# Kernel tuning notes

Hardware: AMD Instinct MI355X
Metric: run time of the kernel (lower is better)

Reference implementation:

```python
import jax, jax.numpy as jnp
import numpy as np

N_TOKENS = 8192
HIDDEN = 4096
N_EXPERTS = 64
TOP_K = 8


def setup_inputs() -> dict:
    key = jax.random.key(0)
    k1, k2 = jax.random.split(key)
    h = jax.random.normal(k1, (N_TOKENS, HIDDEN), dtype=jnp.float32)
    weight = jax.random.normal(k2, (N_EXPERTS, HIDDEN), dtype=jnp.float32) * (1.0 / np.sqrt(HIDDEN))
    return {"h": h, "weight": weight}


def reference(h, weight):
    # logits = h @ W^T in fp32  -> [n_tokens, n_experts]
    logits = jnp.einsum("th,eh->te", h.astype(jnp.float32), weight.astype(jnp.float32))
    scores = jax.nn.softmax(logits, axis=-1)
    topk_weight, topk_idx = jax.lax.top_k(scores, TOP_K)  # [n_tokens, k]
    return topk_weight, topk_idx
```

## Files before the change

### kernel.cpp

```cpp
#include <hip/hip_runtime.h>
#include <math.h>
#include <stdint.h>

#define NTOK 8192
#define HID  4096
#define NEXP 64
#define TOPK 8

typedef float    f32x4 __attribute__((ext_vector_type(4)));
typedef _Float16 f16x8 __attribute__((ext_vector_type(8)));


__device__ __forceinline__ void cvt_hilo(f32x4 a, f32x4 b, f16x8& hi, f16x8& lo)
{
    float x[8] = {a.x, a.y, a.z, a.w, b.x, b.y, b.z, b.w};
#pragma unroll
    for (int j = 0; j < 8; ++j) {
        const _Float16 h = (_Float16)x[j];
        hi[j] = h;
        lo[j] = (_Float16)(x[j] - (float)h);
    }
}

__device__ __forceinline__ void gll16(const void* g, void* l) {
    __builtin_amdgcn_global_load_lds(
        (const __attribute__((address_space(1))) uint32_t*)g,
        (__attribute__((address_space(3))) uint32_t*)l, 16, 0, 0);
}

__global__ __launch_bounds__(256)
void k0_wsplit(const float* __restrict__ W, char* __restrict__ wsW)
{
    const int gidx = blockIdx.x * 256 + threadIdx.x;
    const int kt = gidx >> 9;
    const int r  = (gidx >> 3) & 63;
    const int c  = gidx & 7;

    const float* src = W + (size_t)r * HID + kt * 64 + c * 8;
    const f32x4 w0 = *(const f32x4*)src;
    const f32x4 w1 = *(const f32x4*)(src + 4);
    f16x8 hi, lo;
    cvt_hilo(w0 * 2048.0f, w1 * 2048.0f, hi, lo);

    f16x8* tile = (f16x8*)(wsW + (size_t)kt * 16384);
    const int cp = c ^ (r & 7);
    tile[r * 8 + cp]       = hi;
    tile[512 + r * 8 + cp] = lo;
}

#define AL(SET, S) do { const float* _p = ha + (S) * 32;                      \
    SET##0 = *(const f32x4*)_p; SET##1 = *(const f32x4*)(_p + 4); } while (0)

#define STEPU(SET, KS) do {                                                   \
    f16x8 _ah, _al; cvt_hilo(SET##0, SET##1, _ah, _al);                       \
    const int _ci = ((KS) * 4 + kg) ^ (lr & 7);                               \
    _Pragma("unroll")                                                         \
    for (int _e4 = 0; _e4 < 4; ++_e4) {                                       \
        const int _ix = _e4 * 128 + lr * 8 + _ci;                             \
        const f16x8 _bh = *(const f16x8*)&bt[_ix * 8];                        \
        const f16x8 _bl = *(const f16x8*)&bt[4096 + _ix * 8];                 \
        accH[_e4] = __builtin_amdgcn_mfma_f32_16x16x32_f16(_ah, _bh, accH[_e4], 0, 0, 0); \
        accM[_e4] = __builtin_amdgcn_mfma_f32_16x16x32_f16(_ah, _bl, accM[_e4], 0, 0, 0); \
        accL[_e4] = __builtin_amdgcn_mfma_f32_16x16x32_f16(_al, _bh, accL[_e4], 0, 0, 0); \
    } } while (0)

__global__ __launch_bounds__(256, 3)
void k1_partial(const float* __restrict__ Hm, const char* __restrict__ wsW,
                float* __restrict__ lgp)
{
    __shared__ _Float16 B[2][8192];

    const int tid  = threadIdx.x;
    const int wave = tid >> 6;
    const int l    = tid & 63;
    const int lr   = l & 15;
    const int kg   = l >> 4;
    const int tg   = blockIdx.x >> 2;
    const int m    = blockIdx.x & 3;
    const int tok0 = tg * 64 + wave * 16;

    const float* ha = Hm + (size_t)(tok0 + lr) * HID + m * 1024 + kg * 8;
    const char*  wsrc = wsW + (size_t)m * 16 * 16384 + tid * 16;
    const int    ldsoff = wave * 512;

    f32x4 accH[4], accM[4], accL[4];
#pragma unroll
    for (int e = 0; e < 4; ++e) {
        accH[e] = (f32x4)(0.0f); accM[e] = (f32x4)(0.0f); accL[e] = (f32x4)(0.0f);
    }

    f32x4 Aa0, Aa1, Ab0, Ab1;
    AL(Aa, 0); AL(Ab, 1);
#pragma unroll
    for (int i = 0; i < 4; ++i)
        gll16(wsrc + i * 4096, &B[0][i * 2048 + ldsoff]);
    __syncthreads();

#pragma unroll 1
    for (int kt = 0; kt < 16; ++kt) {
        const int p = kt & 1;
        if (kt < 15) {
            const char* s = wsrc + (size_t)(kt + 1) * 16384;
#pragma unroll
            for (int i = 0; i < 4; ++i)
                gll16(s + i * 4096, &B[p ^ 1][i * 2048 + ldsoff]);
        }
        const _Float16* bt = &B[p][0];
        const int S0 = 2 * kt;
        STEPU(Aa, 0); { const int Sn = (S0 + 2 < 32) ? S0 + 2 : 31; AL(Aa, Sn); }
        STEPU(Ab, 1); { const int Sn = (S0 + 3 < 32) ? S0 + 3 : 31; AL(Ab, Sn); }
        __syncthreads();
    }

    float* wsw = lgp + ((size_t)m * NTOK + tok0) * 64;
#pragma unroll
    for (int e4 = 0; e4 < 4; ++e4) {
        const f32x4 a = accH[e4] + accM[e4] + accL[e4];
#pragma unroll
        for (int r = 0; r < 4; ++r)
            wsw[(kg * 4 + r) * 64 + e4 * 16 + lr] = a[r];
    }
}

__global__ __launch_bounds__(256)
void k2_finish(const float* __restrict__ lgp, float* __restrict__ out)
{
    __shared__ __align__(16) float sc[4][64];
    const int tid  = threadIdx.x;
    const int wave = tid >> 6;
    const int lane = tid & 63;
    float* outw = out;
    float* outi = out + (size_t)NTOK * TOPK;

#pragma unroll 1
    for (int t = 0; t < 4; ++t) {
        const int tok = blockIdx.x * 16 + wave * 4 + t;
        const float* p = lgp + (size_t)tok * 64 + lane;
        const float lgv = ((p[0] + p[(size_t)NTOK * 64])
                         + (p[(size_t)2 * NTOK * 64] + p[(size_t)3 * NTOK * 64]))
                         * (1.0f / 2048.0f);

        float mx = lgv;
#pragma unroll
        for (int off = 32; off; off >>= 1) mx = fmaxf(mx, __shfl_xor(mx, off));
        const float pv = expf(lgv - mx);

        sc[wave][lane] = pv;
        __syncthreads();

        float ss = 0.f;
        int rank = 0;
#pragma unroll
        for (int j4 = 0; j4 < 16; ++j4) {
            const f32x4 v = *(const f32x4*)&sc[wave][j4 * 4];
#pragma unroll
            for (int u = 0; u < 4; ++u) {
                const int j = j4 * 4 + u;
                ss += v[u];
                rank += (v[u] > pv || (v[u] == pv && j < lane)) ? 1 : 0;
            }
        }
        if (rank < TOPK) {
            outw[(size_t)tok * TOPK + rank] = pv / ss;
            outi[(size_t)tok * TOPK + rank] = (float)lane;
        }
        __syncthreads();
    }
}

extern "C" void kernel_launch(void* const* d_in, const int* in_sizes, int n_in,
                              void* d_out, int out_size, void* d_ws, size_t ws_size,
                              hipStream_t stream) {
    (void)in_sizes; (void)n_in; (void)out_size; (void)ws_size;
    const float* h = (const float*)d_in[0];
    const float* w = (const float*)d_in[1];
    float* out = (float*)d_out;

    char*  wsW = (char*)d_ws;
    float* lgp = (float*)((char*)d_ws + (1 << 20));

    k0_wsplit<<<128, 256, 0, stream>>>(w, wsW);
    k1_partial<<<512, 256, 0, stream>>>(h, wsW, lgp);
    k2_finish<<<512, 256, 0, stream>>>(lgp, out);
}
```

Measured before the change: 48.60 us.

## Double K-tile depth, fully unroll k1 with deeper A prefetch, one-token-per-wave finish

After: 44.77 us. 1.09x faster.

```diff
diff --git a/kernel.cpp b/kernel.cpp
--- a/kernel.cpp
+++ b/kernel.cpp
@@ -32,43 +32,61 @@
 void k0_wsplit(const float* __restrict__ W, char* __restrict__ wsW)
 {
     const int gidx = blockIdx.x * 256 + threadIdx.x;
-    const int kt = gidx >> 9;
-    const int r  = (gidx >> 3) & 63;
-    const int c  = gidx & 7;
+    const int kt = gidx >> 10;
+    const int r  = (gidx >> 4) & 63;
+    const int sl = gidx & 15;
+    const int c  = sl ^ (r & 7);
 
-    const float* src = W + (size_t)r * HID + kt * 64 + c * 8;
+    const float* src = W + (size_t)r * HID + kt * 128 + c * 8;
     const f32x4 w0 = *(const f32x4*)src;
     const f32x4 w1 = *(const f32x4*)(src + 4);
     f16x8 hi, lo;
     cvt_hilo(w0 * 2048.0f, w1 * 2048.0f, hi, lo);
 
-    f16x8* tile = (f16x8*)(wsW + (size_t)kt * 16384);
-    const int cp = c ^ (r & 7);
-    tile[r * 8 + cp]       = hi;
-    tile[512 + r * 8 + cp] = lo;
+    f16x8* tile = (f16x8*)(wsW + (size_t)kt * 32768);
+    tile[r * 16 + sl]        = hi;
+    tile[1024 + r * 16 + sl] = lo;
 }
 
 #define AL(SET, S) do { const float* _p = ha + (S) * 32;                      \
     SET##0 = *(const f32x4*)_p; SET##1 = *(const f32x4*)(_p + 4); } while (0)
+#define ALG(SET, S) do { if ((S) < 32) AL(SET, S); } while (0)
 
 #define STEPU(SET, KS) do {                                                   \
     f16x8 _ah, _al; cvt_hilo(SET##0, SET##1, _ah, _al);                       \
-    const int _ci = ((KS) * 4 + kg) ^ (lr & 7);                               \
     _Pragma("unroll")                                                         \
     for (int _e4 = 0; _e4 < 4; ++_e4) {                                       \
-        const int _ix = _e4 * 128 + lr * 8 + _ci;                             \
-        const f16x8 _bh = *(const f16x8*)&bt[_ix * 8];                        \
-        const f16x8 _bl = *(const f16x8*)&bt[4096 + _ix * 8];                 \
+        const int _r  = _e4 * 16 + lr;                                        \
+        const int _sl = ((KS) * 4 + kg) ^ (lr & 7);                           \
+        const f16x8 _bh = *(const f16x8*)&bt[(_r * 16 + _sl) * 8];            \
+        const f16x8 _bl = *(const f16x8*)&bt[8192 + (_r * 16 + _sl) * 8];     \
         accH[_e4] = __builtin_amdgcn_mfma_f32_16x16x32_f16(_ah, _bh, accH[_e4], 0, 0, 0); \
         accM[_e4] = __builtin_amdgcn_mfma_f32_16x16x32_f16(_ah, _bl, accM[_e4], 0, 0, 0); \
         accL[_e4] = __builtin_amdgcn_mfma_f32_16x16x32_f16(_al, _bh, accL[_e4], 0, 0, 0); \
     } } while (0)
 
-__global__ __launch_bounds__(256, 3)
+#define STAGE(KT, BUF) do {                                                   \
+    const char* _s = wsrc + (KT) * 32768;                                     \
+    _Pragma("unroll")                                                         \
+    for (int _t = 0; _t < 8; ++_t)                                            \
+        gll16(_s + _t * 4096, (void*)&BT[BUF][_t * 2048 + tid * 8]);          \
+} while (0)
+
+#define KTILE(KT, SA, SB, SC, SD) do {                                        \
+    if ((KT) < 7) STAGE((KT) + 1, ((KT) & 1) ^ 1);                            \
+    const _Float16* bt = &BT[(KT) & 1][0];                                    \
+    STEPU(SA, 0); ALG(SA, (KT) * 4 + 8);                                      \
+    STEPU(SB, 1); ALG(SB, (KT) * 4 + 9);                                      \
+    STEPU(SC, 2); ALG(SC, (KT) * 4 + 10);                                     \
+    STEPU(SD, 3); ALG(SD, (KT) * 4 + 11);                                     \
+    __syncthreads();                                                          \
+} while (0)
+
+__global__ __launch_bounds__(256, 2)
 void k1_partial(const float* __restrict__ Hm, const char* __restrict__ wsW,
                 float* __restrict__ lgp)
 {
-    __shared__ _Float16 B[2][8192];
+    __shared__ _Float16 BT[2][16384];
 
     const int tid  = threadIdx.x;
     const int wave = tid >> 6;
@@ -79,9 +97,8 @@
     const int m    = blockIdx.x & 3;
     const int tok0 = tg * 64 + wave * 16;
 
-    const float* ha = Hm + (size_t)(tok0 + lr) * HID + m * 1024 + kg * 8;
-    const char*  wsrc = wsW + (size_t)m * 16 * 16384 + tid * 16;
-    const int    ldsoff = wave * 512;
+    const float* ha   = Hm + (size_t)(tok0 + lr) * HID + m * 1024 + kg * 8;
+    const char*  wsrc = wsW + (size_t)m * 8 * 32768 + tid * 16;
 
     f32x4 accH[4], accM[4], accL[4];
 #pragma unroll
@@ -89,28 +106,21 @@
         accH[e] = (f32x4)(0.0f); accM[e] = (f32x4)(0.0f); accL[e] = (f32x4)(0.0f);
     }
 
-    f32x4 Aa0, Aa1, Ab0, Ab1;
-    AL(Aa, 0); AL(Ab, 1);
-#pragma unroll
-    for (int i = 0; i < 4; ++i)
-        gll16(wsrc + i * 4096, &B[0][i * 2048 + ldsoff]);
+    STAGE(0, 0);
+    f32x4 Aa0, Aa1, Ab0, Ab1, Ac0, Ac1, Ad0, Ad1;
+    f32x4 Ae0, Ae1, Af0, Af1, Ag0, Ag1, Ah0, Ah1;
+    AL(Aa, 0); AL(Ab, 1); AL(Ac, 2); AL(Ad, 3);
+    AL(Ae, 4); AL(Af, 5); AL(Ag, 6); AL(Ah, 7);
     __syncthreads();
 
-#pragma unroll 1
-    for (int kt = 0; kt < 16; ++kt) {
-        const int p = kt & 1;
-        if (kt < 15) {
-            const char* s = wsrc + (size_t)(kt + 1) * 16384;
-#pragma unroll
-            for (int i = 0; i < 4; ++i)
-                gll16(s + i * 4096, &B[p ^ 1][i * 2048 + ldsoff]);
-        }
-        const _Float16* bt = &B[p][0];
-        const int S0 = 2 * kt;
-        STEPU(Aa, 0); { const int Sn = (S0 + 2 < 32) ? S0 + 2 : 31; AL(Aa, Sn); }
-        STEPU(Ab, 1); { const int Sn = (S0 + 3 < 32) ? S0 + 3 : 31; AL(Ab, Sn); }
-        __syncthreads();
-    }
+    KTILE(0, Aa, Ab, Ac, Ad);
+    KTILE(1, Ae, Af, Ag, Ah);
+    KTILE(2, Aa, Ab, Ac, Ad);
+    KTILE(3, Ae, Af, Ag, Ah);
+    KTILE(4, Aa, Ab, Ac, Ad);
+    KTILE(5, Ae, Af, Ag, Ah);
+    KTILE(6, Aa, Ab, Ac, Ad);
+    KTILE(7, Ae, Af, Ag, Ah);
 
     float* wsw = lgp + ((size_t)m * NTOK + tok0) * 64;
 #pragma unroll
@@ -132,39 +142,38 @@
     float* outw = out;
     float* outi = out + (size_t)NTOK * TOPK;
 
-#pragma unroll 1
-    for (int t = 0; t < 4; ++t) {
-        const int tok = blockIdx.x * 16 + wave * 4 + t;
-        const float* p = lgp + (size_t)tok * 64 + lane;
-        const float lgv = ((p[0] + p[(size_t)NTOK * 64])
-                         + (p[(size_t)2 * NTOK * 64] + p[(size_t)3 * NTOK * 64]))
-                         * (1.0f / 2048.0f);
+    const int tok = blockIdx.x * 4 + wave;
+    const float* p = lgp + (size_t)tok * 64 + lane;
+    const float lgv = ((p[0] + p[(size_t)NTOK * 64])
+                     + (p[(size_t)2 * NTOK * 64] + p[(size_t)3 * NTOK * 64]))
+                     * (1.0f / 2048.0f);
 
-        float mx = lgv;
+    float mx = lgv;
 #pragma unroll
-        for (int off = 32; off; off >>= 1) mx = fmaxf(mx, __shfl_xor(mx, off));
-        const float pv = expf(lgv - mx);
+    for (int off = 32; off; off >>= 1) mx = fmaxf(mx, __shfl_xor(mx, off));
+    const float pv = expf(lgv - mx);
+    float ss = pv;
+#pragma unroll
+    for (int off = 32; off; off >>= 1) ss += __shfl_xor(ss, off);
+    ss = __shfl(ss, 0);
+    const float sval = pv / ss;
 
-        sc[wave][lane] = pv;
-        __syncthreads();
+    sc[wave][lane] = sval;
+    __syncthreads();
 
-        float ss = 0.f;
-        int rank = 0;
+    int rank = 0;
 #pragma unroll
-        for (int j4 = 0; j4 < 16; ++j4) {
-            const f32x4 v = *(const f32x4*)&sc[wave][j4 * 4];
+    for (int j4 = 0; j4 < 16; ++j4) {
+        const f32x4 v = *(const f32x4*)&sc[wave][j4 * 4];
 #pragma unroll
-            for (int u = 0; u < 4; ++u) {
-                const int j = j4 * 4 + u;
-                ss += v[u];
-                rank += (v[u] > pv || (v[u] == pv && j < lane)) ? 1 : 0;
-            }
+        for (int u = 0; u < 4; ++u) {
+            const int j = j4 * 4 + u;
+            rank += (v[u] > sval || (v[u] == sval && j < lane)) ? 1 : 0;
         }
-        if (rank < TOPK) {
-            outw[(size_t)tok * TOPK + rank] = pv / ss;
-            outi[(size_t)tok * TOPK + rank] = (float)lane;
-        }
-        __syncthreads();
+    }
+    if (rank < TOPK) {
+        outw[(size_t)tok * TOPK + rank] = sval;
+        outi[(size_t)tok * TOPK + rank] = (float)lane;
     }
 }
 
@@ -181,5 +190,5 @@
 
     k0_wsplit<<<128, 256, 0, stream>>>(w, wsW);
     k1_partial<<<512, 256, 0, stream>>>(h, wsW, lgp);
-    k2_finish<<<512, 256, 0, stream>>>(lgp, out);
+    k2_finish<<<NTOK / 4, 256, 0, stream>>>(lgp, out);
 }
```
